# Kernel optimization log

Hardware: AMD Instinct MI355X
Metric: run time of the kernel (lower is better)

Reference implementation:

```python
import jax, jax.numpy as jnp
import numpy as np

B, N, E, F, U = 256, 240, 4338, 28, 100
NEG_SLOPE = 0.2  # PyG GATConv default negative_slope


def setup_inputs() -> dict:
    key = jax.random.key(0)
    ks = jax.random.split(key, 13)
    s = 0.05  # xavier-ish scale
    return {
        "inputs": jax.random.normal(ks[0], (B, N * F), jnp.float32),
        "state": jax.random.normal(ks[1], (B, N * U), jnp.float32),
        "edge_src": jax.random.randint(ks[2], (E,), 0, N, jnp.int32),
        "edge_dst": jax.random.randint(ks[3], (E,), 0, N, jnp.int32),
        # GATConv(U+F -> U): linear weight, attention vectors, output bias
        "Wg": jax.random.normal(ks[4], (U, U + F), jnp.float32) * s,
        "att_src": jax.random.normal(ks[5], (U,), jnp.float32) * s,
        "att_dst": jax.random.normal(ks[6], (U,), jnp.float32) * s,
        "gat_bias": jnp.zeros((U,), jnp.float32),
        # bias_1 added in _gc3 (self.biases[(100,)])
        "bias1": jnp.zeros((U,), jnp.float32),
        # GRU1: GRULinear(100, 200); GRU2: GRULinear(100, 100)
        "W_ru": jax.random.normal(ks[7], (U + F, 2 * U), jnp.float32) * s,
        "b_ru": jnp.zeros((2 * U,), jnp.float32),
        "W_c": jax.random.normal(ks[8], (U + F, U), jnp.float32) * s,
        "b_c": jnp.zeros((U,), jnp.float32),
    }


def _gat_gru(inputs, state, src, dst, Wg, att_src, att_dst, gat_bias, bias1,
             W_ru, b_ru, W_c, b_c):
    xi = inputs.reshape(B, N, F)
    xs = state.reshape(B, N, U)
    # _gc3: concat [state, inputs] -> GATConv per sample (vectorized here)
    x = jnp.concatenate([xs, xi], axis=2)                 # [B, N, U+F]
    h = jnp.einsum("bnf,cf->bnc", x, Wg)                  # [B, N, U]
    a_src = h @ att_src                                    # [B, N]
    a_dst = h @ att_dst                                    # [B, N]
    e = jax.nn.leaky_relu(a_src[:, src] + a_dst[:, dst], NEG_SLOPE)  # [B, E+N]
    eT = e.T                                               # [E+N, B]
    emax = jax.ops.segment_max(eT, dst, num_segments=N)    # [N, B]
    ex = jnp.exp(eT - emax[dst])
    denom = jax.ops.segment_sum(ex, dst, num_segments=N)   # [N, B]
    alpha = ex / denom[dst]                                # [E+N, B]
    msgs = h[:, src].transpose(1, 0, 2) * alpha[:, :, None]  # [E+N, B, U]
    agg = jax.ops.segment_sum(msgs, dst, num_segments=N)   # [N, B, U]
    gstate = agg.transpose(1, 0, 2) + gat_bias + bias1     # [B, N, U]
    st = gstate.reshape(B, N * U)
    # GRU gates (GRULinear concatenates [inputs, hidden] on feature dim)
    cat1 = jnp.concatenate([xi, gstate], axis=2).reshape(-1, U + F)
    ru = jax.nn.sigmoid((cat1 @ W_ru + b_ru).reshape(B, N, 2 * U))
    r = ru[..., :U].reshape(B, N * U)
    u = ru[..., U:].reshape(B, N * U)
    cat2 = jnp.concatenate([xi, (r * st).reshape(B, N, U)], axis=2).reshape(-1, U + F)
    c = jnp.tanh(cat2 @ W_c + b_c).reshape(B, N * U)
    return u * st + (1.0 - u) * c


def reference(inputs, state, edge_src, edge_dst, Wg, att_src, att_dst,
              gat_bias, bias1, W_ru, b_ru, W_c, b_c):
    # PyG GATConv default add_self_loops=True
    loops = jnp.arange(N, dtype=edge_src.dtype)
    src = jnp.concatenate([edge_src, loops])
    dst = jnp.concatenate([edge_dst, loops])
    return _gat_gru(inputs, state, src, dst, Wg, att_src, att_dst, gat_bias,
                    bias1, W_ru, b_ru, W_c, b_c)
```

## Files before the change

kernel.cpp:

```cpp
#include <hip/hip_runtime.h>

#define Bb 256
#define Nn 240
#define Ee 4338
#define Ff 28
#define Uu 100
#define Kk 128
#define AS 136
#define KP 248

typedef __attribute__((ext_vector_type(8))) short bf16x8;
typedef __attribute__((ext_vector_type(4))) float f32x4;
typedef unsigned short u16;

__device__ __forceinline__ float bf2f(u16 u) {
  union { unsigned int i; float f; } v; v.i = ((unsigned int)u) << 16; return v.f;
}
__device__ __forceinline__ u16 f2bf(float f) {
  union { float ff; unsigned int i; } v; v.ff = f;
  unsigned int x = v.i;
  return (u16)((x + 0x7fffu + ((x >> 16) & 1u)) >> 16);
}
__device__ __forceinline__ void split4(const float4 v, ushort4& h, ushort4& l) {
  u16 h0 = f2bf(v.x), h1 = f2bf(v.y), h2 = f2bf(v.z), h3 = f2bf(v.w);
  h.x = h0; h.y = h1; h.z = h2; h.w = h3;
  l.x = f2bf(v.x - bf2f(h0)); l.y = f2bf(v.y - bf2f(h1));
  l.z = f2bf(v.z - bf2f(h2)); l.w = f2bf(v.w - bf2f(h3));
}

__global__ __launch_bounds__(512, 2) void k_fused(
    const float* __restrict__ stt, const float* __restrict__ inp,
    const float* __restrict__ Wg,
    const float* __restrict__ att_s, const float* __restrict__ att_d,
    const int* __restrict__ esrc, const int* __restrict__ edst,
    const float* __restrict__ gbias, const float* __restrict__ b1,
    const float* __restrict__ Wru, const float* __restrict__ bru,
    const float* __restrict__ Wc, const float* __restrict__ bc,
    float* __restrict__ out) {
  __shared__ __align__(16) char smem[154752];
  u16*      hTH    = (u16*)(smem);
  u16*      hTL    = (u16*)(smem + 49600);
  u16*      panel  = (u16*)(smem + 99200);
  u16*      ahL    = panel;
  u16*      alL    = panel + 32 * AS;
  u16*      alphaL = panel;
  float*    gch    = (float*)(smem + 116608);
  unsigned* cntW   = (unsigned*)(smem + 116608);
  u16*      alphaH = (u16*)(smem + 129408);
  u16*      ugQ    = (u16*)(smem + 145280);
  float*    asrcL  = (float*)(smem + 151680);
  float*    adstL  = (float*)(smem + 152640);
  float*    denC   = (float*)(smem + 153600);
  float*    w_asL  = (float*)(smem + 153728);
  float*    w_adL  = (float*)(smem + 154240);

  int tid = threadIdx.x;
  int b = blockIdx.x;
  const size_t sbase = (size_t)b * Nn * Uu;
  const size_t ibase = (size_t)b * Nn * Ff;

  int w = tid >> 6, l = tid & 63, l15 = l & 15, q = l >> 4;
  int cw = w * 16 + l15;

  f32x4 zero = {0.f, 0.f, 0.f, 0.f};
  bf16x8 z8 = {0, 0, 0, 0, 0, 0, 0, 0};

  auto stageChunk = [&](int c0, int rowsn, int base, int stride) {
    for (int j = base; j < rowsn * 32; j += stride) {
      int r = j >> 5, g = j & 31;
      float4 v = (g < 25)
          ? *(const float4*)(stt + sbase + (size_t)(c0 + r) * Uu + g * 4)
          : *(const float4*)(inp + ibase + (size_t)(c0 + r) * Ff + (g - 25) * 4);
      ushort4 hh, lo;
      split4(v, hh, lo);
      *(ushort4*)(ahL + r * AS + g * 4) = hh;
      *(ushort4*)(alL + r * AS + g * 4) = lo;
    }
  };

  if (tid < 256) {
    int k = tid & 127;
    const float* av = (tid < 128) ? att_s : att_d;
    float acc = 0.f;
    for (int c = 0; c < Uu; ++c) acc += Wg[c * Kk + k] * av[c];
    ((tid < 128) ? w_asL : w_adL)[k] = acc;
  } else {
    stageChunk(0, 32, tid - 256, 256);
  }
  __syncthreads();

  {
    bf16x8 wh[4], wl[4];
#pragma unroll
    for (int s = 0; s < 4; ++s) {
#pragma unroll
      for (int j = 0; j < 8; ++j) {
        int kp = s * 32 + q * 8 + j;
        float v = (cw < Uu) ? Wg[cw * Kk + kp]
                : (cw == Uu) ? w_asL[kp]
                : (cw == Uu + 1) ? w_adL[kp] : 0.f;
        u16 hh = f2bf(v);
        wh[s][j] = (short)hh;
        wl[s][j] = (short)f2bf(v - bf2f(hh));
      }
    }

    for (int ch0 = 0; ch0 < Nn; ch0 += 32) {
      int rows = Nn - ch0; if (rows > 32) rows = 32;
      int nrt = rows >> 4;
      f32x4 acc[2]; acc[0] = zero; acc[1] = zero;
#pragma unroll
      for (int rt = 0; rt < 2; ++rt) if (rt < nrt) {
#pragma unroll
        for (int s = 0; s < 4; ++s) {
          bf16x8 a = *(const bf16x8*)(ahL + (rt * 16 + l15) * AS + s * 32 + q * 8);
          bf16x8 bb = *(const bf16x8*)(alL + (rt * 16 + l15) * AS + s * 32 + q * 8);
          acc[rt] = __builtin_amdgcn_mfma_f32_16x16x32_bf16(a, wh[s], acc[rt], 0, 0, 0);
          acc[rt] = __builtin_amdgcn_mfma_f32_16x16x32_bf16(bb, wh[s], acc[rt], 0, 0, 0);
          acc[rt] = __builtin_amdgcn_mfma_f32_16x16x32_bf16(a, wl[s], acc[rt], 0, 0, 0);
        }
      }
#pragma unroll
      for (int rt = 0; rt < 2; ++rt) if (rt < nrt) {
#pragma unroll
        for (int i = 0; i < 4; ++i) {
          float v = acc[rt][i];
          int krow = ch0 + rt * 16 + q * 4 + i;
          if (cw < Uu) {
            u16 hh = f2bf(v);
            hTH[cw * KP + krow] = hh;
            hTL[cw * KP + krow] = f2bf(v - bf2f(hh));
          } else if (cw == Uu) {
            asrcL[krow] = v;
          } else if (cw == Uu + 1) {
            adstL[krow] = v;
          }
        }
      }
      __syncthreads();
      int nx = ch0 + 32;
      if (nx < Nn) {
        int rowsn = Nn - nx; if (rowsn > 32) rowsn = 32;
        stageChunk(nx, rowsn, tid, 512);
      }
      __syncthreads();
    }
  }

  bf16x8 r0h[4], r0l[4], r1h[4], r1l[4], cch[4], ccl[4];
  int cw1 = 128 + cw;
#pragma unroll
  for (int s = 0; s < 4; ++s) {
    int kb = s * 32 + q * 8;
#pragma unroll
    for (int j = 0; j < 8; ++j) {
      int kp = kb + j;
      int k = (kp < Uu) ? (kp + Ff) : (kp - Uu);
      float v0 = Wru[k * (2 * Uu) + cw];
      u16 h0 = f2bf(v0);
      r0h[s][j] = (short)h0; r0l[s][j] = (short)f2bf(v0 - bf2f(h0));
      float v1 = (cw1 < 2 * Uu) ? Wru[k * (2 * Uu) + cw1] : 0.f;
      u16 h1 = f2bf(v1);
      r1h[s][j] = (short)h1; r1l[s][j] = (short)f2bf(v1 - bf2f(h1));
      float v2 = (cw < Uu) ? Wc[k * Uu + cw] : 0.f;
      u16 h2 = f2bf(v2);
      cch[s][j] = (short)h2; ccl[s][j] = (short)f2bf(v2 - bf2f(h2));
    }
  }
  float bru0 = bru[cw];
  float bru1 = (cw1 < 2 * Uu) ? bru[cw1] : 0.f;
  float bcv = (cw < Uu) ? bc[cw] : 0.f;
  int n0 = (w >> 1) * 16 + l15;
  int n1 = (4 + (w >> 1)) * 16 + l15;
  float gb0 = (n0 < Uu) ? gbias[n0] + b1[n0] : 0.f;
  float gb1 = (n1 < Uu) ? gbias[n1] + b1[n1] : 0.f;

  for (int ch0 = 0; ch0 < Nn; ch0 += 32) {
    int rows = Nn - ch0; if (rows > 32) rows = 32;
    int nrt = rows >> 4;

    for (int i = tid; i < 32 * 62; i += 512) cntW[i] = 0;
    __syncthreads();
    for (int e = tid; e < Ee; e += 512) {
      int d = edst[e];
      unsigned r = (unsigned)(d - ch0);
      if (r < 32u) {
        int s = esrc[e];
        atomicAdd(&cntW[r * 62 + (s >> 2)], 1u << (8 * (s & 3)));
      }
    }
    if (tid < rows) {
      int n = ch0 + tid;
      atomicAdd(&cntW[tid * 62 + (n >> 2)], 1u << (8 * (n & 3)));
    }
    __syncthreads();
    {
      int d = tid >> 4, j = tid & 15;
      int gd = ch0 + d;
      float dsum = 0.f;
      if (d < rows) {
        float ad = adstL[gd];
        for (int wi = j; wi < 62; wi += 16) {
          unsigned c4 = cntW[d * 62 + wi];
          ushort4 vh = {0, 0, 0, 0}, vl = {0, 0, 0, 0};
          if (c4) {
#pragma unroll
            for (int bb = 0; bb < 4; ++bb) {
              unsigned c = (c4 >> (8 * bb)) & 0xffu;
              if (c) {
                int s = wi * 4 + bb;
                float sc = asrcL[s] + ad;
                sc = (sc > 0.f) ? sc : 0.2f * sc;
                float we = __expf(sc) * (float)c;
                dsum += we;
                u16 hh = f2bf(we);
                ((u16*)&vh)[bb] = hh;
                ((u16*)&vl)[bb] = f2bf(we - bf2f(hh));
              }
            }
          }
          *(ushort4*)(alphaH + d * KP + wi * 4) = vh;
          *(ushort4*)(alphaL + d * KP + wi * 4) = vl;
        }
      }
      dsum += __shfl_xor(dsum, 1, 16);
      dsum += __shfl_xor(dsum, 2, 16);
      dsum += __shfl_xor(dsum, 4, 16);
      dsum += __shfl_xor(dsum, 8, 16);
      if (j == 0 && d < rows) denC[d] = 1.f / dsum;
    }
    __syncthreads();
#pragma unroll
    for (int p = 0; p < 2; ++p) {
      int mh = w & 1, nt = p * 4 + (w >> 1);
      if (nt > 6 || mh * 16 >= rows) continue;
      int nn = p ? n1 : n0;
      bool bv = (nn < Uu);
      int arow = (mh * 16 + l15) * KP;
      int brow = nn * KP;
      f32x4 acc = zero;
#pragma unroll
      for (int s = 0; s < 8; ++s) {
        int ko = s * 32 + q * 8;
        bool kv = (s < 7) || (q < 2);
        bf16x8 aH = kv ? *(const bf16x8*)(alphaH + arow + ko) : z8;
        bf16x8 aL = kv ? *(const bf16x8*)(alphaL + arow + ko) : z8;
        bf16x8 bH = (kv && bv) ? *(const bf16x8*)(hTH + brow + ko) : z8;
        bf16x8 bL = (kv && bv) ? *(const bf16x8*)(hTL + brow + ko) : z8;
        acc = __builtin_amdgcn_mfma_f32_16x16x32_bf16(aH, bH, acc, 0, 0, 0);
        acc = __builtin_amdgcn_mfma_f32_16x16x32_bf16(aL, bH, acc, 0, 0, 0);
        acc = __builtin_amdgcn_mfma_f32_16x16x32_bf16(aH, bL, acc, 0, 0, 0);
      }
      if (bv) {
        float gb = p ? gb1 : gb0;
#pragma unroll
        for (int i = 0; i < 4; ++i) {
          int m = mh * 16 + q * 4 + i;
          gch[m * Uu + nn] = acc[i] * denC[m] + gb;
        }
      }
    }
    __syncthreads();

    for (int j = tid; j < rows * 32; j += 512) {
      int r = j >> 5, g = j & 31;
      float4 v = (g < 25)
          ? *(const float4*)(gch + r * Uu + g * 4)
          : *(const float4*)(inp + ibase + (size_t)(ch0 + r) * Ff + (g - 25) * 4);
      ushort4 hh, lo;
      split4(v, hh, lo);
      *(ushort4*)(ahL + r * AS + g * 4) = hh;
      *(ushort4*)(alL + r * AS + g * 4) = lo;
    }
    float sv[2][4];
#pragma unroll
    for (int rt = 0; rt < 2; ++rt) if (rt < nrt) {
#pragma unroll
      for (int i = 0; i < 4; ++i) {
        int row = rt * 16 + q * 4 + i;
        sv[rt][i] = (cw < Uu) ? gch[row * Uu + cw] : 0.f;
      }
    }
    __syncthreads();

    float pr[2][4];
    {
      f32x4 acc[2]; acc[0] = zero; acc[1] = zero;
#pragma unroll
      for (int rt = 0; rt < 2; ++rt) if (rt < nrt) {
#pragma unroll
        for (int s = 0; s < 4; ++s) {
          bf16x8 a = *(const bf16x8*)(ahL + (rt * 16 + l15) * AS + s * 32 + q * 8);
          bf16x8 bb = *(const bf16x8*)(alL + (rt * 16 + l15) * AS + s * 32 + q * 8);
          acc[rt] = __builtin_amdgcn_mfma_f32_16x16x32_bf16(a, r0h[s], acc[rt], 0, 0, 0);
          acc[rt] = __builtin_amdgcn_mfma_f32_16x16x32_bf16(bb, r0h[s], acc[rt], 0, 0, 0);
          acc[rt] = __builtin_amdgcn_mfma_f32_16x16x32_bf16(a, r0l[s], acc[rt], 0, 0, 0);
        }
      }
#pragma unroll
      for (int rt = 0; rt < 2; ++rt) if (rt < nrt) {
#pragma unroll
        for (int i = 0; i < 4; ++i) {
          int row = rt * 16 + q * 4 + i;
          float y = acc[rt][i] + bru0;
          float g = 1.f / (1.f + __expf(-y));
          if (cw < Uu) pr[rt][i] = g * sv[rt][i];
          else ugQ[row * Uu + (cw - Uu)] = (u16)(g * 65535.f + 0.5f);
        }
      }
    }
    {
      f32x4 acc[2]; acc[0] = zero; acc[1] = zero;
#pragma unroll
      for (int rt = 0; rt < 2; ++rt) if (rt < nrt) {
#pragma unroll
        for (int s = 0; s < 4; ++s) {
          bf16x8 a = *(const bf16x8*)(ahL + (rt * 16 + l15) * AS + s * 32 + q * 8);
          bf16x8 bb = *(const bf16x8*)(alL + (rt * 16 + l15) * AS + s * 32 + q * 8);
          acc[rt] = __builtin_amdgcn_mfma_f32_16x16x32_bf16(a, r1h[s], acc[rt], 0, 0, 0);
          acc[rt] = __builtin_amdgcn_mfma_f32_16x16x32_bf16(bb, r1h[s], acc[rt], 0, 0, 0);
          acc[rt] = __builtin_amdgcn_mfma_f32_16x16x32_bf16(a, r1l[s], acc[rt], 0, 0, 0);
        }
      }
#pragma unroll
      for (int rt = 0; rt < 2; ++rt) if (rt < nrt) {
#pragma unroll
        for (int i = 0; i < 4; ++i) {
          int row = rt * 16 + q * 4 + i;
          float y = acc[rt][i] + bru1;
          float g = 1.f / (1.f + __expf(-y));
          if (cw1 < 2 * Uu) ugQ[row * Uu + (cw1 - Uu)] = (u16)(g * 65535.f + 0.5f);
        }
      }
    }
    __syncthreads();

#pragma unroll
    for (int rt = 0; rt < 2; ++rt) if (rt < nrt) {
#pragma unroll
      for (int i = 0; i < 4; ++i) {
        int row = rt * 16 + q * 4 + i;
        if (cw < Uu) {
          float p = pr[rt][i];
          u16 hh = f2bf(p);
          ahL[row * AS + cw] = hh;
          alL[row * AS + cw] = f2bf(p - bf2f(hh));
        }
      }
    }
    __syncthreads();

    {
      f32x4 acc[2]; acc[0] = zero; acc[1] = zero;
#pragma unroll
      for (int rt = 0; rt < 2; ++rt) if (rt < nrt) {
#pragma unroll
        for (int s = 0; s < 4; ++s) {
          bf16x8 a = *(const bf16x8*)(ahL + (rt * 16 + l15) * AS + s * 32 + q * 8);
          bf16x8 bb = *(const bf16x8*)(alL + (rt * 16 + l15) * AS + s * 32 + q * 8);
          acc[rt] = __builtin_amdgcn_mfma_f32_16x16x32_bf16(a, cch[s], acc[rt], 0, 0, 0);
          acc[rt] = __builtin_amdgcn_mfma_f32_16x16x32_bf16(bb, cch[s], acc[rt], 0, 0, 0);
          acc[rt] = __builtin_amdgcn_mfma_f32_16x16x32_bf16(a, ccl[s], acc[rt], 0, 0, 0);
        }
      }
#pragma unroll
      for (int rt = 0; rt < 2; ++rt) if (rt < nrt) {
#pragma unroll
        for (int i = 0; i < 4; ++i) {
          int row = rt * 16 + q * 4 + i;
          if (cw < Uu) {
            float y = acc[rt][i] + bcv;
            float cv = 1.f - 2.f / (__expf(2.f * y) + 1.f);
            float u = (float)ugQ[row * Uu + cw] * (1.f / 65535.f);
            out[sbase + (size_t)(ch0 + row) * Uu + cw] = u * sv[rt][i] + (1.f - u) * cv;
          }
        }
      }
    }
    __syncthreads();
  }
}

extern "C" void kernel_launch(void* const* d_in, const int* in_sizes, int n_in,
                              void* d_out, int out_size, void* d_ws, size_t ws_size,
                              hipStream_t stream) {
  const float* inp   = (const float*)d_in[0];
  const float* stt   = (const float*)d_in[1];
  const int*   esrc  = (const int*)d_in[2];
  const int*   edst  = (const int*)d_in[3];
  const float* Wg    = (const float*)d_in[4];
  const float* att_s = (const float*)d_in[5];
  const float* att_d = (const float*)d_in[6];
  const float* gbias = (const float*)d_in[7];
  const float* b1    = (const float*)d_in[8];
  const float* Wru   = (const float*)d_in[9];
  const float* bru   = (const float*)d_in[10];
  const float* Wc    = (const float*)d_in[11];
  const float* bc    = (const float*)d_in[12];
  float* out = (float*)d_out;

  k_fused<<<Bb, 512, 0, stream>>>(stt, inp, Wg, att_s, att_d, esrc, edst,
                                  gbias, b1, Wru, bru, Wc, bc, out);
}
```

Before: 218.3 us.

## Preload packed edge lists into registers and overlap histogram with GRU stages

```diff
diff --git a/kernel.cpp b/kernel.cpp
--- a/kernel.cpp
+++ b/kernel.cpp
@@ -45,7 +45,6 @@
   u16*      alL    = panel + 32 * AS;
   u16*      alphaL = panel;
   float*    gch    = (float*)(smem + 116608);
-  unsigned* cntW   = (unsigned*)(smem + 116608);
   u16*      alphaH = (u16*)(smem + 129408);
   u16*      ugQ    = (u16*)(smem + 145280);
   float*    asrcL  = (float*)(smem + 151680);
@@ -78,6 +77,43 @@
     }
   };
 
+  auto histChunk = [&](int c0, int rowsn, unsigned* epk) {
+    unsigned* cbase = (unsigned*)alphaH;
+#pragma unroll
+    for (int k = 0; k < 5; ++k) {
+      unsigned p = epk[k];
+      {
+        unsigned d = p & 0xFFu, s = (p >> 8) & 0xFFu;
+        unsigned r = d - (unsigned)c0;
+        if (r < (unsigned)rowsn)
+          atomicAdd(&cbase[r * 124 + (s >> 1)], 1u << (16 * (s & 1)));
+      }
+      {
+        unsigned d = (p >> 16) & 0xFFu, s = p >> 24;
+        unsigned r = d - (unsigned)c0;
+        if (r < (unsigned)rowsn)
+          atomicAdd(&cbase[r * 124 + (s >> 1)], 1u << (16 * (s & 1)));
+      }
+    }
+    if (tid < rowsn) {
+      int n = c0 + tid;
+      atomicAdd(&cbase[tid * 124 + (n >> 1)], 1u << (16 * (n & 1)));
+    }
+  };
+
+  unsigned epk[5];
+#pragma unroll
+  for (int k = 0; k < 5; ++k) {
+    int e0 = tid + (2 * k) * 512, e1 = tid + (2 * k + 1) * 512;
+    unsigned d0 = 255u, s0 = 255u, d1 = 255u, s1 = 255u;
+    if (e0 < Ee) { d0 = (unsigned)edst[e0]; s0 = (unsigned)esrc[e0]; }
+    if (e1 < Ee) { d1 = (unsigned)edst[e1]; s1 = (unsigned)esrc[e1]; }
+    epk[k] = d0 | (s0 << 8) | (d1 << 16) | (s1 << 24);
+  }
+  {
+    unsigned* cz = (unsigned*)alphaH;
+    for (int i = tid; i < 32 * 124; i += 512) cz[i] = 0;
+  }
   if (tid < 256) {
     int k = tid & 127;
     const float* av = (tid < 128) ? att_s : att_d;
@@ -147,6 +183,7 @@
     }
   }
 
+  histChunk(0, 32, epk);
   bf16x8 r0h[4], r0l[4], r1h[4], r1l[4], cch[4], ccl[4];
   int cw1 = 128 + cw;
 #pragma unroll
@@ -172,55 +209,49 @@
   float bcv = (cw < Uu) ? bc[cw] : 0.f;
   int n0 = (w >> 1) * 16 + l15;
   int n1 = (4 + (w >> 1)) * 16 + l15;
-  float gb0 = (n0 < Uu) ? gbias[n0] + b1[n0] : 0.f;
-  float gb1 = (n1 < Uu) ? gbias[n1] + b1[n1] : 0.f;
+  __syncthreads();
 
   for (int ch0 = 0; ch0 < Nn; ch0 += 32) {
     int rows = Nn - ch0; if (rows > 32) rows = 32;
     int nrt = rows >> 4;
-
-    for (int i = tid; i < 32 * 62; i += 512) cntW[i] = 0;
-    __syncthreads();
-    for (int e = tid; e < Ee; e += 512) {
-      int d = edst[e];
-      unsigned r = (unsigned)(d - ch0);
-      if (r < 32u) {
-        int s = esrc[e];
-        atomicAdd(&cntW[r * 62 + (s >> 2)], 1u << (8 * (s & 3)));
-      }
-    }
-    if (tid < rows) {
-      int n = ch0 + tid;
-      atomicAdd(&cntW[tid * 62 + (n >> 2)], 1u << (8 * (n & 3)));
-    }
-    __syncthreads();
+    int nx = ch0 + 32;
+    int rows_nx = (nx < Nn) ? ((Nn - nx > 32) ? 32 : (Nn - nx)) : 0;
+
     {
       int d = tid >> 4, j = tid & 15;
-      int gd = ch0 + d;
       float dsum = 0.f;
       if (d < rows) {
-        float ad = adstL[gd];
-        for (int wi = j; wi < 62; wi += 16) {
-          unsigned c4 = cntW[d * 62 + wi];
-          ushort4 vh = {0, 0, 0, 0}, vl = {0, 0, 0, 0};
-          if (c4) {
-#pragma unroll
-            for (int bb = 0; bb < 4; ++bb) {
-              unsigned c = (c4 >> (8 * bb)) & 0xffu;
-              if (c) {
-                int s = wi * 4 + bb;
-                float sc = asrcL[s] + ad;
-                sc = (sc > 0.f) ? sc : 0.2f * sc;
-                float we = __expf(sc) * (float)c;
-                dsum += we;
-                u16 hh = f2bf(we);
-                ((u16*)&vh)[bb] = hh;
-                ((u16*)&vl)[bb] = f2bf(we - bf2f(hh));
-              }
+        float ad = adstL[ch0 + d];
+        unsigned* crow = (unsigned*)(alphaH + d * KP);
+        unsigned* lrow = (unsigned*)(alphaL + d * KP);
+        for (int wd = j; wd < 120; wd += 16) {
+          unsigned c2 = crow[wd];
+          unsigned hi2 = 0, lo2 = 0;
+          if (c2) {
+            unsigned ca = c2 & 0xFFFFu, cb = c2 >> 16;
+            if (ca) {
+              int s = 2 * wd;
+              float sc = asrcL[s] + ad;
+              sc = (sc > 0.f) ? sc : 0.2f * sc;
+              float we = __expf(sc) * (float)ca;
+              dsum += we;
+              u16 hh = f2bf(we);
+              hi2 |= (unsigned)hh;
+              lo2 |= (unsigned)f2bf(we - bf2f(hh));
+            }
+            if (cb) {
+              int s = 2 * wd + 1;
+              float sc = asrcL[s] + ad;
+              sc = (sc > 0.f) ? sc : 0.2f * sc;
+              float we = __expf(sc) * (float)cb;
+              dsum += we;
+              u16 hh = f2bf(we);
+              hi2 |= ((unsigned)hh) << 16;
+              lo2 |= ((unsigned)f2bf(we - bf2f(hh))) << 16;
             }
           }
-          *(ushort4*)(alphaH + d * KP + wi * 4) = vh;
-          *(ushort4*)(alphaL + d * KP + wi * 4) = vl;
+          crow[wd] = hi2;
+          lrow[wd] = lo2;
         }
       }
       dsum += __shfl_xor(dsum, 1, 16);
@@ -230,6 +261,7 @@
       if (j == 0 && d < rows) denC[d] = 1.f / dsum;
     }
     __syncthreads();
+
 #pragma unroll
     for (int p = 0; p < 2; ++p) {
       int mh = w & 1, nt = p * 4 + (w >> 1);
@@ -252,7 +284,7 @@
         acc = __builtin_amdgcn_mfma_f32_16x16x32_bf16(aH, bL, acc, 0, 0, 0);
       }
       if (bv) {
-        float gb = p ? gb1 : gb0;
+        float gb = gbias[nn] + b1[nn];
 #pragma unroll
         for (int i = 0; i < 4; ++i) {
           int m = mh * 16 + q * 4 + i;
@@ -272,6 +304,10 @@
       *(ushort4*)(ahL + r * AS + g * 4) = hh;
       *(ushort4*)(alL + r * AS + g * 4) = lo;
     }
+    if (rows_nx) {
+      unsigned* cz = (unsigned*)alphaH;
+      for (int i = tid; i < 32 * 124; i += 512) cz[i] = 0;
+    }
     float sv[2][4];
 #pragma unroll
     for (int rt = 0; rt < 2; ++rt) if (rt < nrt) {
@@ -348,6 +384,7 @@
         }
       }
     }
+    if (rows_nx) histChunk(nx, rows_nx, epk);
     __syncthreads();
 
     {
```

New measurement: 213.7 us. 2.1% less time.
